# Kernel tuning notes

Hardware: AMD Instinct MI355X
Metric: run time of the kernel (lower is better)

Reference implementation:

```python
import jax, jax.numpy as jnp
import numpy as np

B, S, D, N = 128, 1024, 512, 784  # batch, state_dim, image_feature_dim, spatial positions


def setup_inputs() -> dict:
    key = jax.random.key(0)
    ks = jax.random.split(key, 6)
    s = lambda fan_in: 1.0 / np.sqrt(fan_in)
    return {
        "in_state": jax.random.normal(ks[0], (B, S), jnp.float32),
        "image": jax.random.normal(ks[1], (B, D, N), jnp.float32),
        "Wq": jax.random.normal(ks[2], (D, S), jnp.float32) * s(S),
        "bq": jnp.zeros((D,), jnp.float32),
        "Wc": jax.random.normal(ks[3], (D, 2 * D), jnp.float32) * s(2 * D),
        "bc": jnp.zeros((D,), jnp.float32),
        "Wa": jax.random.normal(ks[4], (1, D), jnp.float32) * s(D),
        "ba": jnp.zeros((1,), jnp.float32),
        "Wo": jax.random.normal(ks[5], (S, D), jnp.float32) * s(D),
        "bo": jnp.zeros((S,), jnp.float32),
    }


def reference(in_state, image, Wq, bq, Wc, bc, Wa, ba, Wo, bo):
    # query: [B, D]
    query = in_state @ Wq.T + bq
    # broadcast multiply over spatial positions: [B, D, N]
    qimg = query[:, :, None] * image
    # cat along channel dim then permute -> [B, N, 2D]
    feats = jnp.concatenate([qimg, image], axis=1).transpose(0, 2, 1)
    # concat linear: [B, N, D]
    c = feats @ Wc.T + bc
    # attention logits: [B, N]
    logits = (c @ Wa.T + ba)[..., 0]
    attn = jax.nn.softmax(logits, axis=1)  # softmax over spatial dim
    # weighted sum over spatial positions: [B, D]
    pooled = jnp.einsum("bn,bdn->bd", attn, image)
    return pooled @ Wo.T + bo
```

## Files before the change

### kernel.cpp

```cpp
#include <hip/hip_runtime.h>
#include <math.h>

#define BB 128
#define SS 1024
#define DD 512
#define NN 784
#define NCHK 4
#define NC 196

__device__ __forceinline__ float wave_reduce_sum(float x) {
#pragma unroll
  for (int m = 32; m > 0; m >>= 1) x += __shfl_xor(x, m, 64);
  return x;
}
__device__ __forceinline__ float wave_reduce_max(float x) {
#pragma unroll
  for (int m = 32; m > 0; m >>= 1) x = fmaxf(x, __shfl_xor(x, m, 64));
  return x;
}

__global__ void k1_v(const float* __restrict__ Wa, const float* __restrict__ Wc,
                     float* __restrict__ v) {
  int k = blockIdx.x * 256 + threadIdx.x;
  int j0 = blockIdx.y * 32;
  float acc = 0.f;
#pragma unroll
  for (int j = 0; j < 32; ++j)
    acc += Wa[j0 + j] * Wc[(size_t)(j0 + j) * (2 * DD) + k];
  atomicAdd(&v[k], acc);
}

__global__ void k2_w(const float* __restrict__ in_state, const float* __restrict__ Wq,
                     const float* __restrict__ bq, const float* __restrict__ v,
                     float* __restrict__ w) {
  __shared__ float st[SS];
  int b = blockIdx.y;
  int t = threadIdx.x, lane = t & 63, wv = t >> 6;
  ((float4*)st)[t] = ((const float4*)(in_state + (size_t)b * SS))[t];
  __syncthreads();
  const float4* st4 = (const float4*)st;
  float4 s0 = st4[lane], s1 = st4[lane + 64], s2 = st4[lane + 128], s3 = st4[lane + 192];
  int d0 = blockIdx.x * 32 + wv * 8;
  float acc[8];
#pragma unroll
  for (int r = 0; r < 8; ++r) {
    const float4* q4 = (const float4*)(Wq + (size_t)(d0 + r) * SS);
    float4 a0 = q4[lane], a1 = q4[lane + 64], a2 = q4[lane + 128], a3 = q4[lane + 192];
    acc[r] = a0.x * s0.x + a0.y * s0.y + a0.z * s0.z + a0.w * s0.w
           + a1.x * s1.x + a1.y * s1.y + a1.z * s1.z + a1.w * s1.w
           + a2.x * s2.x + a2.y * s2.y + a2.z * s2.z + a2.w * s2.w
           + a3.x * s3.x + a3.y * s3.y + a3.z * s3.z + a3.w * s3.w;
  }
#pragma unroll
  for (int r = 0; r < 8; ++r) acc[r] = wave_reduce_sum(acc[r]);
  if (lane == 0) {
#pragma unroll
    for (int r = 0; r < 8; ++r) {
      int d = d0 + r;
      w[(size_t)b * DD + d] = (acc[r] + bq[d]) * v[d] + v[DD + d];
    }
  }
}

__global__ void k3_fused(const float* __restrict__ image, const float* __restrict__ w,
                         float* __restrict__ P_part, float* __restrict__ mZ_part) {
  __shared__ float w_lds[DD];
  __shared__ float4 red[8][49];
  __shared__ float4 u_lds[49];
  __shared__ float p_s[DD];
  int b = blockIdx.y, c = blockIdx.x;
  int t = threadIdx.x, lane = t & 63, wv = t >> 6;
  w_lds[t] = w[(size_t)b * DD + t];
  __syncthreads();
  const float4* img4 = (const float4*)image + (size_t)b * DD * 196;
  int d0 = wv * 64;
  const float4* pbase = img4 + (size_t)d0 * 196 + c * 49 + (lane < 49 ? lane : 48);
  float4 acc = {0, 0, 0, 0};
#pragma unroll 8
  for (int i = 0; i < 64; ++i) {
    float4 x = pbase[i * 196];
    float wd = w_lds[d0 + i];
    acc.x += wd * x.x; acc.y += wd * x.y; acc.z += wd * x.z; acc.w += wd * x.w;
  }
  if (lane < 49) red[wv][lane] = acc;
  __syncthreads();
  if (wv == 0) {
    float4 l4 = {0, 0, 0, 0};
    float lm = -1e30f;
    if (lane < 49) {
#pragma unroll
      for (int v8 = 0; v8 < 8; ++v8) {
        float4 r = red[v8][lane];
        l4.x += r.x; l4.y += r.y; l4.z += r.z; l4.w += r.w;
      }
      lm = fmaxf(fmaxf(l4.x, l4.y), fmaxf(l4.z, l4.w));
    }
    float m = wave_reduce_max(lm);
    float zs = 0.f;
    if (lane < 49) {
      float4 u4;
      u4.x = __expf(l4.x - m); u4.y = __expf(l4.y - m);
      u4.z = __expf(l4.z - m); u4.w = __expf(l4.w - m);
      zs = u4.x + u4.y + u4.z + u4.w;
      u_lds[lane] = u4;
    }
    float Z = wave_reduce_sum(zs);
    if (lane == 0) {
      mZ_part[((size_t)b * NCHK + c) * 2 + 0] = m;
      mZ_part[((size_t)b * NCHK + c) * 2 + 1] = Z;
    }
  }
  __syncthreads();
  float4 u4 = {0, 0, 0, 0};
  if (lane < 49) u4 = u_lds[lane];
#pragma unroll 4
  for (int i = 0; i < 64; ++i) {
    float part = 0.f;
    if (lane < 49) {
      float4 x = pbase[i * 196];
      part = u4.x * x.x + u4.y * x.y + u4.z * x.z + u4.w * x.w;
    }
    part = wave_reduce_sum(part);
    if (lane == 0) p_s[d0 + i] = part;
  }
  P_part[((size_t)b * NCHK + c) * DD + d0 + lane] = p_s[d0 + lane];
}

__global__ void k5_combine(const float* __restrict__ P_part, const float* __restrict__ mZ_part,
                           float* __restrict__ pooled) {
  int b = blockIdx.x, t = threadIdx.x;
  float mc[NCHK], Zc[NCHK];
  float M = -1e30f;
#pragma unroll
  for (int c = 0; c < NCHK; ++c) {
    mc[c] = mZ_part[((size_t)b * NCHK + c) * 2 + 0];
    Zc[c] = mZ_part[((size_t)b * NCHK + c) * 2 + 1];
    M = fmaxf(M, mc[c]);
  }
  float Z = 0.f, al[NCHK];
#pragma unroll
  for (int c = 0; c < NCHK; ++c) { al[c] = __expf(mc[c] - M); Z += al[c] * Zc[c]; }
  float inv = 1.0f / Z;
  float4 s = {0, 0, 0, 0};
#pragma unroll
  for (int c = 0; c < NCHK; ++c) {
    float4 p = ((const float4*)P_part)[((size_t)b * NCHK + c) * 128 + t];
    s.x += al[c] * p.x; s.y += al[c] * p.y; s.z += al[c] * p.z; s.w += al[c] * p.w;
  }
  s.x *= inv; s.y *= inv; s.z *= inv; s.w *= inv;
  ((float4*)pooled)[(size_t)b * 128 + t] = s;
}

__global__ void k6_out(const float* __restrict__ pooled, const float* __restrict__ Wo,
                       const float* __restrict__ bo, float* __restrict__ out) {
  __shared__ float p_s[DD];
  int b = blockIdx.y, t = threadIdx.x, lane = t & 63, wv = t >> 6;
  ((float2*)p_s)[t] = ((const float2*)(pooled + (size_t)b * DD))[t];
  __syncthreads();
  const float4* p4 = (const float4*)p_s;
  float4 p0 = p4[lane], p1 = p4[lane + 64];
  int s0 = blockIdx.x * 32 + wv * 8;
  float acc[8];
#pragma unroll
  for (int r = 0; r < 8; ++r) {
    const float4* wo4 = (const float4*)(Wo + (size_t)(s0 + r) * DD);
    float4 x0 = wo4[lane], x1 = wo4[lane + 64];
    acc[r] = x0.x * p0.x + x0.y * p0.y + x0.z * p0.z + x0.w * p0.w
           + x1.x * p1.x + x1.y * p1.y + x1.z * p1.z + x1.w * p1.w;
  }
#pragma unroll
  for (int r = 0; r < 8; ++r) acc[r] = wave_reduce_sum(acc[r]);
  if (lane == 0) {
#pragma unroll
    for (int r = 0; r < 8; ++r) out[(size_t)b * SS + s0 + r] = acc[r] + bo[s0 + r];
  }
}

extern "C" void kernel_launch(void* const* d_in, const int* in_sizes, int n_in,
                              void* d_out, int out_size, void* d_ws, size_t ws_size,
                              hipStream_t stream) {
  const float* in_state = (const float*)d_in[0];
  const float* image    = (const float*)d_in[1];
  const float* Wq       = (const float*)d_in[2];
  const float* bq       = (const float*)d_in[3];
  const float* Wc       = (const float*)d_in[4];
  const float* Wa       = (const float*)d_in[6];
  const float* Wo       = (const float*)d_in[8];
  const float* bo       = (const float*)d_in[9];
  float* out = (float*)d_out;

  float* ws      = (float*)d_ws;
  float* v       = ws;
  float* w       = v + 2 * DD;
  float* P_part  = w + BB * DD;
  float* mZ_part = P_part + (size_t)BB * NCHK * DD;
  float* pooled  = mZ_part + (size_t)BB * NCHK * 2;

  hipMemsetAsync(v, 0, 2 * DD * sizeof(float), stream);
  k1_v<<<dim3(4, 16), 256, 0, stream>>>(Wa, Wc, v);
  k2_w<<<dim3(16, BB), 256, 0, stream>>>(in_state, Wq, bq, v, w);
  k3_fused<<<dim3(NCHK, BB), 512, 0, stream>>>(image, w, P_part, mZ_part);
  k5_combine<<<BB, 128, 0, stream>>>(P_part, mZ_part, pooled);
  k6_out<<<dim3(32, BB), 256, 0, stream>>>(pooled, Wo, bo, out);
}
```

Before: 372.7 us.

## Cache image tile in registers for both passes and fuse combine into output GEMV

```diff
diff --git a/kernel.cpp b/kernel.cpp
--- a/kernel.cpp
+++ b/kernel.cpp
@@ -65,22 +65,25 @@
 __global__ void k3_fused(const float* __restrict__ image, const float* __restrict__ w,
                          float* __restrict__ P_part, float* __restrict__ mZ_part) {
   __shared__ float w_lds[DD];
-  __shared__ float4 red[8][49];
+  __shared__ float4 red[16][49];
   __shared__ float4 u_lds[49];
   __shared__ float p_s[DD];
   int b = blockIdx.y, c = blockIdx.x;
   int t = threadIdx.x, lane = t & 63, wv = t >> 6;
-  w_lds[t] = w[(size_t)b * DD + t];
-  __syncthreads();
-  const float4* img4 = (const float4*)image + (size_t)b * DD * 196;
-  int d0 = wv * 64;
-  const float4* pbase = img4 + (size_t)d0 * 196 + c * 49 + (lane < 49 ? lane : 48);
+  if (t < DD) w_lds[t] = w[(size_t)b * DD + t];
+  __syncthreads();
+  const float4* img4 = (const float4*)image + (size_t)b * DD * 49 * NCHK;
+  int d0 = wv * 32;
+  const float4* pbase = img4 + (size_t)d0 * (49 * NCHK) + c * 49 + (lane < 49 ? lane : 48);
+  float4 x[32];
+#pragma unroll
+  for (int i = 0; i < 32; ++i) x[i] = pbase[(size_t)i * (49 * NCHK)];
   float4 acc = {0, 0, 0, 0};
-#pragma unroll 8
-  for (int i = 0; i < 64; ++i) {
-    float4 x = pbase[i * 196];
+#pragma unroll
+  for (int i = 0; i < 32; ++i) {
     float wd = w_lds[d0 + i];
-    acc.x += wd * x.x; acc.y += wd * x.y; acc.z += wd * x.z; acc.w += wd * x.w;
+    acc.x += wd * x[i].x; acc.y += wd * x[i].y;
+    acc.z += wd * x[i].z; acc.w += wd * x[i].w;
   }
   if (lane < 49) red[wv][lane] = acc;
   __syncthreads();
@@ -89,8 +92,8 @@
     float lm = -1e30f;
     if (lane < 49) {
 #pragma unroll
-      for (int v8 = 0; v8 < 8; ++v8) {
-        float4 r = red[v8][lane];
+      for (int v16 = 0; v16 < 16; ++v16) {
+        float4 r = red[v16][lane];
         l4.x += r.x; l4.y += r.y; l4.z += r.z; l4.w += r.w;
       }
       lm = fmaxf(fmaxf(l4.x, l4.y), fmaxf(l4.z, l4.w));
@@ -113,22 +116,23 @@
   __syncthreads();
   float4 u4 = {0, 0, 0, 0};
   if (lane < 49) u4 = u_lds[lane];
-#pragma unroll 4
-  for (int i = 0; i < 64; ++i) {
+#pragma unroll
+  for (int i = 0; i < 32; ++i) {
     float part = 0.f;
-    if (lane < 49) {
-      float4 x = pbase[i * 196];
-      part = u4.x * x.x + u4.y * x.y + u4.z * x.z + u4.w * x.w;
-    }
+    if (lane < 49)
+      part = u4.x * x[i].x + u4.y * x[i].y + u4.z * x[i].z + u4.w * x[i].w;
     part = wave_reduce_sum(part);
     if (lane == 0) p_s[d0 + i] = part;
   }
-  P_part[((size_t)b * NCHK + c) * DD + d0 + lane] = p_s[d0 + lane];
-}
-
-__global__ void k5_combine(const float* __restrict__ P_part, const float* __restrict__ mZ_part,
-                           float* __restrict__ pooled) {
-  int b = blockIdx.x, t = threadIdx.x;
+  __syncthreads();
+  if (t < DD) P_part[((size_t)b * NCHK + c) * DD + t] = p_s[t];
+}
+
+__global__ void k6_out(const float* __restrict__ P_part, const float* __restrict__ mZ_part,
+                       const float* __restrict__ Wo, const float* __restrict__ bo,
+                       float* __restrict__ out) {
+  __shared__ float p_s[DD];
+  int b = blockIdx.y, t = threadIdx.x, lane = t & 63, wv = t >> 6;
   float mc[NCHK], Zc[NCHK];
   float M = -1e30f;
 #pragma unroll
@@ -141,21 +145,16 @@
 #pragma unroll
   for (int c = 0; c < NCHK; ++c) { al[c] = __expf(mc[c] - M); Z += al[c] * Zc[c]; }
   float inv = 1.0f / Z;
-  float4 s = {0, 0, 0, 0};
-#pragma unroll
-  for (int c = 0; c < NCHK; ++c) {
-    float4 p = ((const float4*)P_part)[((size_t)b * NCHK + c) * 128 + t];
-    s.x += al[c] * p.x; s.y += al[c] * p.y; s.z += al[c] * p.z; s.w += al[c] * p.w;
-  }
-  s.x *= inv; s.y *= inv; s.z *= inv; s.w *= inv;
-  ((float4*)pooled)[(size_t)b * 128 + t] = s;
-}
-
-__global__ void k6_out(const float* __restrict__ pooled, const float* __restrict__ Wo,
-                       const float* __restrict__ bo, float* __restrict__ out) {
-  __shared__ float p_s[DD];
-  int b = blockIdx.y, t = threadIdx.x, lane = t & 63, wv = t >> 6;
-  ((float2*)p_s)[t] = ((const float2*)(pooled + (size_t)b * DD))[t];
+  {
+    float2 s = {0, 0};
+    const float2* pp = (const float2*)(P_part + (size_t)b * NCHK * DD);
+#pragma unroll
+    for (int c = 0; c < NCHK; ++c) {
+      float2 p = pp[c * (DD / 2) + t];
+      s.x += al[c] * p.x; s.y += al[c] * p.y;
+    }
+    ((float2*)p_s)[t] = make_float2(s.x * inv, s.y * inv);
+  }
   __syncthreads();
   const float4* p4 = (const float4*)p_s;
   float4 p0 = p4[lane], p1 = p4[lane + 64];
@@ -194,12 +193,10 @@
   float* w       = v + 2 * DD;
   float* P_part  = w + BB * DD;
   float* mZ_part = P_part + (size_t)BB * NCHK * DD;
-  float* pooled  = mZ_part + (size_t)BB * NCHK * 2;
 
   hipMemsetAsync(v, 0, 2 * DD * sizeof(float), stream);
   k1_v<<<dim3(4, 16), 256, 0, stream>>>(Wa, Wc, v);
   k2_w<<<dim3(16, BB), 256, 0, stream>>>(in_state, Wq, bq, v, w);
-  k3_fused<<<dim3(NCHK, BB), 512, 0, stream>>>(image, w, P_part, mZ_part);
-  k5_combine<<<BB, 128, 0, stream>>>(P_part, mZ_part, pooled);
-  k6_out<<<dim3(32, BB), 256, 0, stream>>>(pooled, Wo, bo, out);
-}
+  k3_fused<<<dim3(NCHK, BB), 1024, 0, stream>>>(image, w, P_part, mZ_part);
+  k6_out<<<dim3(32, BB), 256, 0, stream>>>(P_part, mZ_part, Wo, bo, out);
+}
```

After: 377.7 us. No clear change (+1.3%).
